# Optimization experiments

Hardware: AMD Instinct MI355X
Metric: run time of the kernel (lower is better)

Reference implementation:

```python
import jax, jax.numpy as jnp
import numpy as np
import math

N = 512  # num particles
D = 128  # particle dimension


def setup_inputs() -> dict:
    key = jax.random.key(0)
    particles = jax.random.normal(key, (N, D), dtype=jnp.float32)
    return {"particles": particles}


def reference(particles):
    # particles: [N, D]
    n = particles.shape[0]
    # delta_x[i, j] = particles[j] - particles[i]  (matches unsqueeze(0) - unsqueeze(1))
    delta_x = particles[None, :, :] - particles[:, None, :]   # [N, N, D]
    norm_sq = delta_x * delta_x                               # [N, N, D]

    # mode='univ': per-dimension median over strictly-upper-triangular pairs
    iu_r, iu_c = np.triu_indices(n, k=1)                      # static indices
    sel = norm_sq[iu_r, iu_c, :]                              # [M, D], M = N(N-1)/2
    m = sel.shape[0]
    # torch.median returns the LOWER of the two middle values for even counts
    median = jnp.sort(sel, axis=0)[(m - 1) // 2]              # [D]

    h = median / math.log(n + 1)
    bandwidth = jnp.maximum(h, jnp.asarray(1e-9, dtype=h.dtype))  # [D]

    log_kernel = -(norm_sq / bandwidth)                       # [N, N, D]
    grad_log_kernel = -2.0 * delta_x / bandwidth              # [N, N, D]
    return log_kernel, grad_log_kernel
```

## Files before the change

### kernel.cpp

```cpp
#include <hip/hip_runtime.h>
#include <hip/hip_bf16.h>

#define NP 512
#define DD 128
#define NPAIRS (NP * (NP - 1) / 2)

__device__ __forceinline__ float bitonic512(float r, int tid, float* lds)
{
    for (int k = 2; k <= NP; k <<= 1) {
        for (int s = k >> 1; s > 0; s >>= 1) {
            float other;
            if (s < 64) {
                other = __shfl_xor(r, s);
            } else {
                __syncthreads();
                lds[tid] = r;
                __syncthreads();
                other = lds[tid ^ s];
            }
            const bool lower = (tid & s) == 0;
            const bool up    = (tid & k) == 0;
            r = (lower == up) ? fminf(r, other) : fmaxf(r, other);
        }
    }
    return r;
}

__global__ void __launch_bounds__(512)
median_bw_kernel(const float* __restrict__ particles, float* __restrict__ inv_bw)
{
    const int d = blockIdx.x, tid = threadIdx.x, lane = tid & 63, wid = tid >> 6;

    __shared__ float v[NP];
    __shared__ float cand[NP];
    __shared__ int   cnt_s[2][8];
    __shared__ float sum_s[8];
    __shared__ int   scan_s[8];

    float r = particles[tid * DD + d];
    r = bitonic512(r, tid, v);
    __syncthreads();
    v[tid] = r;
    __syncthreads();

    const float vj = r;
    const int want1 = (NPAIRS - 1) / 2 + 1;

    float s = (tid >= 150) ? (vj - v[tid - 150]) : 0.0f;
    #pragma unroll
    for (int off = 32; off > 0; off >>= 1) s += __shfl_xor(s, off);
    if (lane == 0) sum_s[wid] = s;
    __syncthreads();
    float msum = 0.0f;
    #pragma unroll
    for (int w = 0; w < 8; ++w) msum += sum_s[w];
    const float meanp = fmaxf(msum / 362.0f, 0.0f);

    const float maxd = v[NP - 1] - v[0];
    unsigned lo = 0u;
    unsigned hi = __float_as_uint(maxd) + 1u;
    int C_lo = 0;
    int C_hi = NPAIRS;
    int A = 0, B = tid;
    int buf = 0, round = 0;

    while (lo < hi) {
        if (C_hi - C_lo <= NP) break;

        unsigned mid;
        if (round == 0) {
            mid = __float_as_uint(0.93f * meanp);
        } else if (round == 1) {
            mid = __float_as_uint(1.07f * meanp);
        } else {
            const float flo = __uint_as_float(lo);
            const float fhi = __uint_as_float(hi);
            mid = __float_as_uint(0.5f * (flo + fhi));
        }
        if (mid < lo)      mid = lo;
        if (mid > hi - 1u) mid = hi - 1u;
        const float x = __uint_as_float(mid);

        int a = A, b = B;
        while (a < b) {
            const int   m  = (a + b) >> 1;
            const float pv = v[m];
            const bool  t  = (vj - pv <= x);
            b = t ? m : b;
            a = t ? a : m + 1;
        }
        int cnt = tid - a;

        #pragma unroll
        for (int off = 32; off > 0; off >>= 1) cnt += __shfl_xor(cnt, off);
        if (lane == 0) cnt_s[buf][wid] = cnt;
        __syncthreads();
        int tot = 0;
        #pragma unroll
        for (int w = 0; w < 8; ++w) tot += cnt_s[buf][w];

        if (tot >= want1) { hi = mid;      C_hi = tot; A = a; }
        else              { lo = mid + 1u; C_lo = tot; B = a; }
        buf ^= 1;
        ++round;
    }

    if (lo >= hi) {
        if (tid == 0) {
            const float Dk = __uint_as_float(lo);
            const float h  = (Dk * Dk) / 6.240275844172107f;
            inv_bw[d] = 1.0f / fmaxf(h, 1e-9f);
        }
    } else {
        const int T  = C_hi - C_lo;
        const int rr = min(want1 - C_lo, T);
        const int n  = B - A;
        int inc = n;
        #pragma unroll
        for (int off = 1; off < 64; off <<= 1) {
            const int t = __shfl_up(inc, off);
            if (lane >= off) inc += t;
        }
        if (lane == 63) scan_s[wid] = inc;
        __syncthreads();
        int woff = 0;
        #pragma unroll
        for (int w = 0; w < 8; ++w) woff += (w < wid) ? scan_s[w] : 0;
        int off0 = woff + inc - n;
        for (int i = A; i < B; ++i) cand[off0++] = vj - v[i];
        __syncthreads();

        float c = (tid < T) ? cand[tid] : INFINITY;
        c = bitonic512(c, tid, v);

        if (tid == rr - 1) {
            const float Dk = c;
            const float h  = (Dk * Dk) / 6.240275844172107f;
            inv_bw[d] = 1.0f / fmaxf(h, 1e-9f);
        }
    }
}

__global__ void __launch_bounds__(256)
stein_out_kernel(const float* __restrict__ particles,
                 const float* __restrict__ inv_bw,
                 float4* __restrict__ out_lk,
                 float4* __restrict__ out_g)
{
    const float4* __restrict__ p4  = (const float4*)particles;
    const float4* __restrict__ ib4 = (const float4*)inv_bw;
    const int total = NP * NP * (DD / 4);

    for (int t = blockIdx.x * blockDim.x + threadIdx.x; t < total;
         t += gridDim.x * blockDim.x) {
        const int d4 = t & (DD / 4 - 1);
        const int j  = (t >> 5) & (NP - 1);
        const int i  = t >> 14;

        const float4 xj = p4[j * (DD / 4) + d4];
        const float4 xi = p4[i * (DD / 4) + d4];
        const float4 ib = ib4[d4];

        float4 lk, g;
        {
            const float dx = xj.x - xi.x;
            lk.x = -(dx * dx * ib.x);
            g.x  = -2.0f * dx * ib.x;
        }
        {
            const float dx = xj.y - xi.y;
            lk.y = -(dx * dx * ib.y);
            g.y  = -2.0f * dx * ib.y;
        }
        {
            const float dx = xj.z - xi.z;
            lk.z = -(dx * dx * ib.z);
            g.z  = -2.0f * dx * ib.z;
        }
        {
            const float dx = xj.w - xi.w;
            lk.w = -(dx * dx * ib.w);
            g.w  = -2.0f * dx * ib.w;
        }
        out_lk[t] = lk;
        out_g[t]  = g;
    }
}

extern "C" void kernel_launch(void* const* d_in, const int* in_sizes, int n_in,
                              void* d_out, int out_size, void* d_ws, size_t ws_size,
                              hipStream_t stream)
{
    const float* particles = (const float*)d_in[0];
    float* out    = (float*)d_out;
    float* inv_bw = (float*)d_ws;

    median_bw_kernel<<<DD, 512, 0, stream>>>(particles, inv_bw);

    float4* out_lk = (float4*)out;
    float4* out_g  = (float4*)(out + (size_t)NP * NP * DD);
    stein_out_kernel<<<2048, 256, 0, stream>>>(particles, inv_bw, out_lk, out_g);
}
```

Before: 64.22 us.

## Use count-interpolated bisection, rank-count selection, and single-stream output writes

The median search now picks its pivot by interpolating between the known counts at lo and hi, aiming about 240 ranks past the target, and falls back to plain bisection every fourth round. The goal is fewer passes over the binary-search counts. The final candidate bitonic sort is replaced by a direct rank count: each thread counts how many candidates are less than and equal to its value, using float4 LDS reads. The output kernel now walks one contiguous index space covering both output tensors, so each thread writes one float4 per iteration instead of two streams. That halves the work per iteration, but the difference and the loads are recomputed for each half.

```diff
diff --git a/kernel.cpp b/kernel.cpp
--- a/kernel.cpp
+++ b/kernel.cpp
@@ -32,7 +32,7 @@
     const int d = blockIdx.x, tid = threadIdx.x, lane = tid & 63, wid = tid >> 6;
 
     __shared__ float v[NP];
-    __shared__ float cand[NP];
+    __shared__ __align__(16) float cand[NP];
     __shared__ int   cnt_s[2][8];
     __shared__ float sum_s[8];
     __shared__ int   scan_s[8];
@@ -72,10 +72,18 @@
             mid = __float_as_uint(0.93f * meanp);
         } else if (round == 1) {
             mid = __float_as_uint(1.07f * meanp);
+        } else if ((round & 3) == 3) {
+            mid = lo + ((hi - lo) >> 1);
         } else {
-            const float flo = __uint_as_float(lo);
-            const float fhi = __uint_as_float(hi);
-            mid = __float_as_uint(0.5f * (flo + fhi));
+            const int upslack = C_hi - want1;
+            const int dnslack = want1 - 1 - C_lo;
+            int target = (upslack >= dnslack) ? (want1 + 240) : (want1 - 240);
+            if (target <= C_lo) target = C_lo + 1;
+            if (target >  C_hi) target = C_hi;
+            const float frac = (float)(target - C_lo) / (float)(C_hi - C_lo);
+            const float flo  = __uint_as_float(lo);
+            const float fhi  = __uint_as_float(hi);
+            mid = __float_as_uint(flo + (fhi - flo) * frac);
         }
         if (mid < lo)      mid = lo;
         if (mid > hi - 1u) mid = hi - 1u;
@@ -115,6 +123,7 @@
         const int T  = C_hi - C_lo;
         const int rr = min(want1 - C_lo, T);
         const int n  = B - A;
+        cand[tid] = INFINITY;
         int inc = n;
         #pragma unroll
         for (int off = 1; off < 64; off <<= 1) {
@@ -130,10 +139,16 @@
         for (int i = A; i < B; ++i) cand[off0++] = vj - v[i];
         __syncthreads();
 
-        float c = (tid < T) ? cand[tid] : INFINITY;
-        c = bitonic512(c, tid, v);
-
-        if (tid == rr - 1) {
+        const float c = cand[tid];
+        int cl = 0, ce = 0;
+        const float4* c4 = (const float4*)cand;
+        #pragma unroll 4
+        for (int k4 = 0; k4 < NP / 4; ++k4) {
+            const float4 q = c4[k4];
+            cl += (q.x <  c) + (q.y <  c) + (q.z <  c) + (q.w <  c);
+            ce += (q.x == c) + (q.y == c) + (q.z == c) + (q.w == c);
+        }
+        if (tid < T && cl < rr && rr <= cl + ce) {
             const float Dk = c;
             const float h  = (Dk * Dk) / 6.240275844172107f;
             inv_bw[d] = 1.0f / fmaxf(h, 1e-9f);
@@ -144,15 +159,16 @@
 __global__ void __launch_bounds__(256)
 stein_out_kernel(const float* __restrict__ particles,
                  const float* __restrict__ inv_bw,
-                 float4* __restrict__ out_lk,
-                 float4* __restrict__ out_g)
+                 float4* __restrict__ out)
 {
     const float4* __restrict__ p4  = (const float4*)particles;
     const float4* __restrict__ ib4 = (const float4*)inv_bw;
-    const int total = NP * NP * (DD / 4);
-
-    for (int t = blockIdx.x * blockDim.x + threadIdx.x; t < total;
-         t += gridDim.x * blockDim.x) {
+    const int half = NP * NP * (DD / 4);
+
+    for (int u = blockIdx.x * blockDim.x + threadIdx.x; u < 2 * half;
+         u += gridDim.x * blockDim.x) {
+        const bool isg = (u >= half);
+        const int t  = isg ? u - half : u;
         const int d4 = t & (DD / 4 - 1);
         const int j  = (t >> 5) & (NP - 1);
         const int i  = t >> 14;
@@ -161,29 +177,24 @@
         const float4 xi = p4[i * (DD / 4) + d4];
         const float4 ib = ib4[d4];
 
-        float4 lk, g;
-        {
-            const float dx = xj.x - xi.x;
-            lk.x = -(dx * dx * ib.x);
-            g.x  = -2.0f * dx * ib.x;
-        }
-        {
-            const float dx = xj.y - xi.y;
-            lk.y = -(dx * dx * ib.y);
-            g.y  = -2.0f * dx * ib.y;
-        }
-        {
-            const float dx = xj.z - xi.z;
-            lk.z = -(dx * dx * ib.z);
-            g.z  = -2.0f * dx * ib.z;
-        }
-        {
-            const float dx = xj.w - xi.w;
-            lk.w = -(dx * dx * ib.w);
-            g.w  = -2.0f * dx * ib.w;
-        }
-        out_lk[t] = lk;
-        out_g[t]  = g;
+        const float dx0 = xj.x - xi.x;
+        const float dx1 = xj.y - xi.y;
+        const float dx2 = xj.z - xi.z;
+        const float dx3 = xj.w - xi.w;
+
+        float4 o;
+        if (!isg) {
+            o.x = -(dx0 * dx0 * ib.x);
+            o.y = -(dx1 * dx1 * ib.y);
+            o.z = -(dx2 * dx2 * ib.z);
+            o.w = -(dx3 * dx3 * ib.w);
+        } else {
+            o.x = -2.0f * dx0 * ib.x;
+            o.y = -2.0f * dx1 * ib.y;
+            o.z = -2.0f * dx2 * ib.z;
+            o.w = -2.0f * dx3 * ib.w;
+        }
+        out[u] = o;
     }
 }
 
@@ -196,8 +207,5 @@
     float* inv_bw = (float*)d_ws;
 
     median_bw_kernel<<<DD, 512, 0, stream>>>(particles, inv_bw);
-
-    float4* out_lk = (float4*)out;
-    float4* out_g  = (float4*)(out + (size_t)NP * NP * DD);
-    stein_out_kernel<<<2048, 256, 0, stream>>>(particles, inv_bw, out_lk, out_g);
-}
+    stein_out_kernel<<<2048, 256, 0, stream>>>(particles, inv_bw, (float4*)out);
+}
```

After: 72.26 us. 1.13x slower.
